# Kernel tuning notes

Hardware: AMD Instinct MI355X
Metric: run time of the kernel (lower is better)

Reference implementation:

```python
import jax, jax.numpy as jnp
import numpy as np

NUM_LAYERS = 3

def setup_inputs() -> dict:
    key = jax.random.key(0)
    ks = jax.random.split(key, 16)
    B = 8192
    NU, NI, D = 60000, 40000, 64
    N = NU + NI
    T_TRAIN, T_MAX = 128, 256
    E = 1600000
    return {
        "user_indices": jax.random.randint(ks[0], (B,), 0, NU, dtype=jnp.int32).astype(jnp.int64),
        "item_indices": jax.random.randint(ks[1], (B,), 0, NI, dtype=jnp.int32).astype(jnp.int64),
        "time_diffs": jax.random.randint(ks[2], (B,), 0, T_TRAIN, dtype=jnp.int32).astype(jnp.int64),
        "user_trends": jax.random.normal(ks[3], (B, T_TRAIN), dtype=jnp.float32),
        "item_trends": jax.random.normal(ks[4], (B, T_TRAIN), dtype=jnp.float32),
        "user_emb_table": 0.01 * jax.random.normal(ks[5], (NU, D), dtype=jnp.float32),
        "item_emb_table": 0.01 * jax.random.normal(ks[6], (NI, D), dtype=jnp.float32),
        "user_time_table": 0.01 * jax.random.normal(ks[7], (NU, T_MAX), dtype=jnp.float32),
        "item_time_table": 0.01 * jax.random.normal(ks[8], (NI, T_MAX), dtype=jnp.float32),
        "W1": 0.05 * jax.random.normal(ks[9], (T_TRAIN, 32), dtype=jnp.float32),
        "b1": jnp.zeros((32,), dtype=jnp.float32),
        "W2": 0.05 * jax.random.normal(ks[10], (32, T_MAX - T_TRAIN), dtype=jnp.float32),
        "b2": jnp.zeros((T_MAX - T_TRAIN,), dtype=jnp.float32),
        "edge_src": jax.random.randint(ks[11], (E,), 0, N, dtype=jnp.int32),
        "edge_dst": jax.random.randint(ks[12], (E,), 0, N, dtype=jnp.int32),
    }


def _graph_forward(user_emb_table, item_emb_table, edge_src, edge_dst):
    # LightGCN-style: mean of in-neighbor source features, num_layers hops,
    # then average over [input, layer1, ..., layerL] embeddings.
    N = user_emb_table.shape[0] + item_emb_table.shape[0]
    emb = jnp.concatenate([user_emb_table, item_emb_table], axis=0)  # [N, D]
    deg = jax.ops.segment_sum(jnp.ones_like(edge_dst, dtype=emb.dtype), edge_dst, num_segments=N)
    inv_deg = jnp.where(deg > 0, 1.0 / jnp.maximum(deg, 1.0), 0.0)[:, None]  # zero for isolated nodes (DGL mean -> 0)
    acc = emb
    cur = emb
    for _ in range(NUM_LAYERS):
        msgs = cur[edge_src]  # [E, D] gather
        summed = jax.ops.segment_sum(msgs, edge_dst, num_segments=N)
        cur = summed * inv_deg
        acc = acc + cur
    final = acc / jnp.asarray(NUM_LAYERS + 1, emb.dtype)
    return final[: user_emb_table.shape[0]], final[user_emb_table.shape[0]:]


def _mlp(t, W1, b1, W2, b2):
    # Linear->ReLU->Dropout(eval: identity)->Linear
    h = jax.nn.relu(t @ W1 + b1)
    return h @ W2 + b2


def reference(user_indices, item_indices, time_diffs, user_trends, item_trends,
              user_emb_table, item_emb_table, user_time_table, item_time_table,
              W1, b1, W2, b2, edge_src, edge_dst):
    user_embeddings, item_embeddings = _graph_forward(user_emb_table, item_emb_table, edge_src, edge_dst)
    ue = user_embeddings[user_indices]  # [B, D]
    ie = item_embeddings[item_indices]  # [B, D]
    global_match = jnp.sum(ue * ie, axis=-1)  # [B]

    ute = user_time_table[user_indices]  # [B, T_MAX]
    ite = item_time_table[item_indices]
    ut = jnp.concatenate([user_trends, _mlp(user_trends, W1, b1, W2, b2)], axis=1)  # [B, T_MAX]
    it = jnp.concatenate([item_trends, _mlp(item_trends, W1, b1, W2, b2)], axis=1)
    user_time_match = jnp.sum(ute * ut, axis=-1)
    item_time_match = jnp.sum(ite * it, axis=-1)

    B = user_indices.shape[0]
    ue0 = user_emb_table[user_indices]
    ie0 = item_emb_table[item_indices]
    reg_loss = 0.5 * (jnp.sum(ue0 ** 2) + jnp.sum(ie0 ** 2) + jnp.sum(ute ** 2) + jnp.sum(ite ** 2)) / float(B)

    return (jax.nn.sigmoid(global_match), jax.nn.sigmoid(user_time_match + item_time_match), reg_loss)
```

## Files before the change

### kernel.cpp

```cpp
#include <hip/hip_runtime.h>
#include <math.h>


__device__ __forceinline__ float bf2f(unsigned short h) {
    return __uint_as_float((unsigned)h << 16);
}
__device__ __forceinline__ unsigned short f2bf(float f) {
    unsigned u = __float_as_uint(f);
    return (unsigned short)((u + 0x7fffu + ((u >> 16) & 1u)) >> 16);
}


__global__ __launch_bounds__(256) void conv_kernel(
    const float* __restrict__ utab, const float* __restrict__ itab,
    unsigned short* __restrict__ fb, int total, int uElems,
    int* __restrict__ cursor2, float* __restrict__ out2, int convBlocks) {
    if ((int)blockIdx.x == convBlocks) {
        cursor2[threadIdx.x] = 0;
        if (threadIdx.x == 0) out2[0] = 0.0f;
        return;
    }
    int i = (blockIdx.x * 256 + threadIdx.x) * 4;
    if (i >= total + 64) return;
    ushort4 o;
    if (i < total) {
        const float* srcp = (i < uElems) ? (utab + i) : (itab + (i - uElems));
        float4 v = *(const float4*)srcp;
        o.x = f2bf(v.x); o.y = f2bf(v.y); o.z = f2bf(v.z); o.w = f2bf(v.w);
    } else {
        o.x = 0; o.y = 0; o.z = 0; o.w = 0;
    }
    *(ushort4*)(fb + i) = o;
}


__global__ __launch_bounds__(256) void bin2_kernel(
    const int* __restrict__ src, const int* __restrict__ dst,
    int* __restrict__ cursor2, unsigned long long* __restrict__ pairs2,
    int E, int cap) {
    __shared__ int lcnt[256];
    __shared__ int lbase[256];
    int tid = threadIdx.x;
    int base = blockIdx.x * 4096;
    lcnt[tid] = 0;
    __syncthreads();
    #pragma unroll
    for (int i = 0; i < 16; ++i) {
        int e = base + i * 256 + tid;
        if (e < E) atomicAdd(&lcnt[dst[e] >> 9], 1);
    }
    __syncthreads();
    int c = lcnt[tid];
    lbase[tid] = (c > 0) ? atomicAdd(&cursor2[tid], c) : 0;
    __syncthreads();
    lcnt[tid] = 0;
    __syncthreads();
    #pragma unroll
    for (int i = 0; i < 16; ++i) {
        int e = base + i * 256 + tid;
        if (e < E) {
            int d = dst[e], s = src[e];
            int b = d >> 9;
            int r = lbase[b] + atomicAdd(&lcnt[b], 1);
            if (r < cap)
                pairs2[(size_t)b * cap + r] =
                    ((unsigned long long)(unsigned)d << 32) | (unsigned)s;
        }
    }
}


__global__ __launch_bounds__(256) void sort3_kernel(
    const unsigned long long* __restrict__ pairs2,
    const int* __restrict__ cursor2,
    float* __restrict__ invd, int* __restrict__ csr, int NODE_N, int cap) {
    __shared__ int lcnt[512];
    int bin = blockIdx.x;
    int nodebase = bin << 9;
    int n = cursor2[bin];
    if (n > cap) n = cap;
    const unsigned long long* p = pairs2 + (size_t)bin * cap;
    int tid = threadIdx.x;

    lcnt[tid] = 0;
    lcnt[tid + 256] = 0;
    __syncthreads();
    for (int i = tid; i < n; i += 256) {
        unsigned long long pr = p[i];
        int d = (int)(pr >> 32), s = (int)(pr & 0xffffffffu);
        int pos = atomicAdd(&lcnt[d - nodebase], 1);
        if (pos < 64) csr[(size_t)d * 64 + pos] = s;
    }
    __syncthreads();
    #pragma unroll
    for (int t = 0; t < 2; ++t) {
        int j = tid + t * 256;
        int node = nodebase + j;
        if (node <= NODE_N) {
            int own = lcnt[j];
            invd[node] = (own > 0) ? 1.0f / (float)own : 0.0f;
            int d0 = (own < 64) ? own : 64;
            int pend = (own <= 32) ? 32 : 64;
            int* row = csr + (size_t)node * 64;
            for (int k = d0; k < pend; ++k) row[k] = NODE_N;
        }
    }
}


#define GATHER4(buf, sv, gx, gy, gz, gw_)                                  \
    {                                                                      \
        ushort4 v_ = *(const ushort4*)((buf) + (size_t)(sv) * 64 + 4 * cL);\
        gx += bf2f(v_.x); gy += bf2f(v_.y);                                \
        gz += bf2f(v_.z); gw_ += bf2f(v_.w);                               \
    }
#define RED2(x) { x += __shfl_xor(x, 16, 64); x += __shfl_xor(x, 32, 64); }

__global__ __launch_bounds__(256) void prop_kernel(
    const unsigned short* __restrict__ cur,
    const int* __restrict__ csr, const float* __restrict__ invd,
    unsigned short* __restrict__ nxt, int NP1) {
    int w = (blockIdx.x * blockDim.x + threadIdx.x) >> 6;
    int lane = threadIdx.x & 63;
    int n0 = 2 * w, n1 = 2 * w + 1;
    if (n0 >= NP1) return;
    bool v1 = (n1 < NP1);
    int n1c = v1 ? n1 : n0;
    int g = lane >> 4;
    int cL = lane & 15;
    const int* c0 = csr + (size_t)n0 * 64;
    const int* c1 = csr + (size_t)n1c * 64;
    float inv0 = invd[n0];
    float inv1 = v1 ? invd[n1c] : 0.f;
    int s0 = c0[g], s1 = c0[4 + g], s2 = c0[8 + g], s3 = c0[12 + g];
    int t0 = c1[g], t1 = c1[4 + g], t2 = c1[8 + g], t3 = c1[12 + g];

    float ax = 0.f, ay = 0.f, az = 0.f, aw = 0.f;
    float bx = 0.f, by = 0.f, bz = 0.f, bw = 0.f;
    float ex = 0.f, ey = 0.f, ez = 0.f, ew = 0.f;
    float fx = 0.f, fy = 0.f, fz = 0.f, fw = 0.f;
    GATHER4(cur, s0, ax, ay, az, aw);
    GATHER4(cur, s1, bx, by, bz, bw);
    GATHER4(cur, t0, ex, ey, ez, ew);
    GATHER4(cur, t1, fx, fy, fz, fw);
    GATHER4(cur, s2, ax, ay, az, aw);
    GATHER4(cur, s3, bx, by, bz, bw);
    GATHER4(cur, t2, ex, ey, ez, ew);
    GATHER4(cur, t3, fx, fy, fz, fw);

    int deg0 = (inv0 > 0.f) ? (int)(1.0f / inv0 + 0.5f) : 0;
    int deg1 = (inv1 > 0.f) ? (int)(1.0f / inv1 + 0.5f) : 0;
    if (deg0 > 16) {
        int s4 = c0[16 + g], s5 = c0[20 + g], s6 = c0[24 + g], s7 = c0[28 + g];
        GATHER4(cur, s4, ax, ay, az, aw);
        GATHER4(cur, s5, bx, by, bz, bw);
        GATHER4(cur, s6, ax, ay, az, aw);
        GATHER4(cur, s7, bx, by, bz, bw);
    }
    if (deg1 > 16) {
        int t4 = c1[16 + g], t5 = c1[20 + g], t6 = c1[24 + g], t7 = c1[28 + g];
        GATHER4(cur, t4, ex, ey, ez, ew);
        GATHER4(cur, t5, fx, fy, fz, fw);
        GATHER4(cur, t6, ex, ey, ez, ew);
        GATHER4(cur, t7, fx, fy, fz, fw);
    }
    if (deg0 > 32) {
        #pragma unroll
        for (int pb = 32; pb < 64; pb += 8) {
            int u0 = c0[pb + g], u1 = c0[pb + 4 + g];
            GATHER4(cur, u0, ax, ay, az, aw);
            GATHER4(cur, u1, bx, by, bz, bw);
        }
    }
    if (deg1 > 32) {
        #pragma unroll
        for (int pb = 32; pb < 64; pb += 8) {
            int u0 = c1[pb + g], u1 = c1[pb + 4 + g];
            GATHER4(cur, u0, ex, ey, ez, ew);
            GATHER4(cur, u1, fx, fy, fz, fw);
        }
    }
    ax += bx; ay += by; az += bz; aw += bw;
    ex += fx; ey += fy; ez += fz; ew += fw;
    RED2(ax); RED2(ay); RED2(az); RED2(aw);
    RED2(ex); RED2(ey); RED2(ez); RED2(ew);
    if (g == 0) {
        ushort4 o;
        o.x = f2bf(ax * inv0); o.y = f2bf(ay * inv0);
        o.z = f2bf(az * inv0); o.w = f2bf(aw * inv0);
        *(ushort4*)(nxt + (size_t)n0 * 64 + 4 * cL) = o;
    } else if (g == 1 && v1) {
        ushort4 o;
        o.x = f2bf(ex * inv1); o.y = f2bf(ey * inv1);
        o.z = f2bf(ez * inv1); o.w = f2bf(ew * inv1);
        *(ushort4*)(nxt + (size_t)n1c * 64 + 4 * cL) = o;
    }
}


__global__ __launch_bounds__(256) void timedot_kernel(
    const int* __restrict__ uidx, const int* __restrict__ iidx,
    const float* __restrict__ utr, const float* __restrict__ itr,
    const float* __restrict__ utt, const float* __restrict__ itt,
    const float* __restrict__ utab, const float* __restrict__ itab,
    const float* __restrict__ W1, const float* __restrict__ b1,
    const float* __restrict__ W2, const float* __restrict__ b2,
    const unsigned short* __restrict__ fb2,
    const unsigned short* __restrict__ fb1l,
    const int* __restrict__ csr, const float* __restrict__ invd,
    float* __restrict__ out0, float* __restrict__ out1,
    float* __restrict__ out2, int B, int NU, float regScale) {
    __shared__ float sh[4][320];
    __shared__ float rsh[4];
    int wid = threadIdx.x >> 6, lane = threadIdx.x & 63;
    int b = blockIdx.x * 4 + wid;
    bool valid = (b < B);
    int bb = valid ? b : (B - 1);

    float* tu = sh[wid];
    float* ti = tu + 128;
    float* hu = ti + 128;
    float* hi = hu + 32;

    tu[lane]      = utr[(size_t)bb * 128 + lane];
    tu[lane + 64] = utr[(size_t)bb * 128 + 64 + lane];
    ti[lane]      = itr[(size_t)bb * 128 + lane];
    ti[lane + 64] = itr[(size_t)bb * 128 + 64 + lane];
    __syncthreads();

    {
        int j = lane & 31;
        const float* t = (lane < 32) ? tu : ti;
        float acc = b1[j];
        #pragma unroll 8
        for (int k = 0; k < 128; ++k) acc += t[k] * W1[k * 32 + j];
        float* h = (lane < 32) ? hu : hi;
        h[j] = fmaxf(acc, 0.0f);
    }
    __syncthreads();

    float mu0 = b2[lane], mu1 = b2[64 + lane];
    float mi0 = b2[lane], mi1 = b2[64 + lane];
    #pragma unroll 8
    for (int j = 0; j < 32; ++j) {
        float w0 = W2[j * 128 + lane], w1 = W2[j * 128 + 64 + lane];
        float huj = hu[j], hij = hi[j];
        mu0 += huj * w0; mu1 += huj * w1;
        mi0 += hij * w0; mi1 += hij * w1;
    }

    int u = uidx[bb], it = iidx[bb];
    const float* uterow = utt + (size_t)u * 256;
    const float* iterow = itt + (size_t)it * 256;
    float ute0 = uterow[lane], ute1 = uterow[64 + lane], ute2 = uterow[128 + lane], ute3 = uterow[192 + lane];
    float ite0 = iterow[lane], ite1 = iterow[64 + lane], ite2 = iterow[128 + lane], ite3 = iterow[192 + lane];

    float utm = ute0 * tu[lane] + ute1 * tu[64 + lane] + ute2 * mu0 + ute3 * mu1;
    float itm = ite0 * ti[lane] + ite1 * ti[64 + lane] + ite2 * mi0 + ite3 * mi1;

    float regA = ute0 * ute0 + ute1 * ute1 + ute2 * ute2 + ute3 * ute3
               + ite0 * ite0 + ite1 * ite1 + ite2 * ite2 + ite3 * ite3;

    int g = lane >> 4;
    int cL = lane & 15;
    int nu_node = u;
    int ni_node = NU + it;
    const int* cu = csr + (size_t)nu_node * 64;
    const int* ci = csr + (size_t)ni_node * 64;
    float invU = invd[nu_node];
    float invI = invd[ni_node];
    int s0 = cu[g], s1 = cu[4 + g], s2 = cu[8 + g], s3 = cu[12 + g];
    int s4 = cu[16 + g], s5 = cu[20 + g], s6 = cu[24 + g], s7 = cu[28 + g];
    int t0 = ci[g], t1 = ci[4 + g], t2 = ci[8 + g], t3 = ci[12 + g];
    int t4 = ci[16 + g], t5 = ci[20 + g], t6 = ci[24 + g], t7 = ci[28 + g];

    float ax = 0.f, ay = 0.f, az = 0.f, aw = 0.f;
    float bx = 0.f, by = 0.f, bz = 0.f, bw = 0.f;
    float ex = 0.f, ey = 0.f, ez = 0.f, ew = 0.f;
    float fx = 0.f, fy = 0.f, fz = 0.f, fw = 0.f;
    GATHER4(fb2, s0, ax, ay, az, aw);
    GATHER4(fb2, s1, bx, by, bz, bw);
    GATHER4(fb2, t0, ex, ey, ez, ew);
    GATHER4(fb2, t1, fx, fy, fz, fw);
    GATHER4(fb2, s2, ax, ay, az, aw);
    GATHER4(fb2, s3, bx, by, bz, bw);
    GATHER4(fb2, t2, ex, ey, ez, ew);
    GATHER4(fb2, t3, fx, fy, fz, fw);
    GATHER4(fb2, s4, ax, ay, az, aw);
    GATHER4(fb2, s5, bx, by, bz, bw);
    GATHER4(fb2, t4, ex, ey, ez, ew);
    GATHER4(fb2, t5, fx, fy, fz, fw);
    GATHER4(fb2, s6, ax, ay, az, aw);
    GATHER4(fb2, s7, bx, by, bz, bw);
    GATHER4(fb2, t6, ex, ey, ez, ew);
    GATHER4(fb2, t7, fx, fy, fz, fw);

    int degU = (invU > 0.f) ? (int)(1.0f / invU + 0.5f) : 0;
    int degI = (invI > 0.f) ? (int)(1.0f / invI + 0.5f) : 0;
    if (degU > 32) {
        #pragma unroll
        for (int pb = 32; pb < 64; pb += 8) {
            int u0 = cu[pb + g], u1 = cu[pb + 4 + g];
            GATHER4(fb2, u0, ax, ay, az, aw);
            GATHER4(fb2, u1, bx, by, bz, bw);
        }
    }
    if (degI > 32) {
        #pragma unroll
        for (int pb = 32; pb < 64; pb += 8) {
            int u0 = ci[pb + g], u1 = ci[pb + 4 + g];
            GATHER4(fb2, u0, ex, ey, ez, ew);
            GATHER4(fb2, u1, fx, fy, fz, fw);
        }
    }
    ax += bx; ay += by; az += bz; aw += bw;
    ex += fx; ey += fy; ez += fz; ew += fw;
    RED2(ax); RED2(ay); RED2(az); RED2(aw);
    RED2(ex); RED2(ey); RED2(ez); RED2(ew);

    float4 l0u = *(const float4*)(utab + (size_t)nu_node * 64 + 4 * cL);
    float4 l0i = *(const float4*)(itab + (size_t)it * 64 + 4 * cL);
    ushort4 l1u = *(const ushort4*)(fb1l + (size_t)nu_node * 64 + 4 * cL);
    ushort4 l1i = *(const ushort4*)(fb1l + (size_t)ni_node * 64 + 4 * cL);
    ushort4 l2u = *(const ushort4*)(fb2 + (size_t)nu_node * 64 + 4 * cL);
    ushort4 l2i = *(const ushort4*)(fb2 + (size_t)ni_node * 64 + 4 * cL);

    float ue0_ = l0u.x + bf2f(l1u.x) + bf2f(l2u.x) + ax * invU;
    float ue1_ = l0u.y + bf2f(l1u.y) + bf2f(l2u.y) + ay * invU;
    float ue2_ = l0u.z + bf2f(l1u.z) + bf2f(l2u.z) + az * invU;
    float ue3_ = l0u.w + bf2f(l1u.w) + bf2f(l2u.w) + aw * invU;
    float ie0_ = l0i.x + bf2f(l1i.x) + bf2f(l2i.x) + ex * invI;
    float ie1_ = l0i.y + bf2f(l1i.y) + bf2f(l2i.y) + ey * invI;
    float ie2_ = l0i.z + bf2f(l1i.z) + bf2f(l2i.z) + ez * invI;
    float ie3_ = l0i.w + bf2f(l1i.w) + bf2f(l2i.w) + ew * invI;

    float dv = ue0_ * ie0_ + ue1_ * ie1_ + ue2_ * ie2_ + ue3_ * ie3_;
    float regB = l0u.x * l0u.x + l0u.y * l0u.y + l0u.z * l0u.z + l0u.w * l0u.w
               + l0i.x * l0i.x + l0i.y * l0i.y + l0i.z * l0i.z + l0i.w * l0i.w;
    float reg = regA + 0.25f * regB;

    float s = utm + itm;
    for (int o = 32; o; o >>= 1) {
        s   += __shfl_down(s, o, 64);
        reg += __shfl_down(reg, o, 64);
        dv  += __shfl_down(dv, o, 64);
    }
    if (lane == 0) {
        if (valid) {
            out0[b] = 1.0f / (1.0f + expf(-dv * (1.0f / 64.0f)));
            out1[b] = 1.0f / (1.0f + expf(-s));
        }
        rsh[wid] = valid ? reg : 0.0f;
    }
    __syncthreads();
    if (threadIdx.x == 0) {
        float blocksum = rsh[0] + rsh[1] + rsh[2] + rsh[3];
        atomicAdd(out2, blocksum * regScale);
    }
}

extern "C" void kernel_launch(void* const* d_in, const int* in_sizes, int n_in,
                              void* d_out, int out_size, void* d_ws, size_t ws_size,
                              hipStream_t stream) {
    const int*   uidx = (const int*)d_in[0];
    const int*   iidx = (const int*)d_in[1];
    const float* utr  = (const float*)d_in[3];
    const float* itr  = (const float*)d_in[4];
    const float* utab = (const float*)d_in[5];
    const float* itab = (const float*)d_in[6];
    const float* utt  = (const float*)d_in[7];
    const float* itt  = (const float*)d_in[8];
    const float* W1   = (const float*)d_in[9];
    const float* b1   = (const float*)d_in[10];
    const float* W2   = (const float*)d_in[11];
    const float* b2   = (const float*)d_in[12];
    const int*   esrc = (const int*)d_in[13];
    const int*   edst = (const int*)d_in[14];

    const int B  = in_sizes[0];
    const int H  = in_sizes[10];
    const int TT = in_sizes[9] / H;
    const int TM = TT + in_sizes[12];
    const int NU = in_sizes[7] / TM;
    const int NI = in_sizes[8] / TM;
    const int N  = NU + NI;
    const int E  = in_sizes[13];
    const int D  = 64;
    const int nbin = (N + 1 + 511) >> 9;
    const int cap = 12288;

    char* ws = (char*)d_ws;
    size_t o = 0;
    auto carve = [&](size_t bytes) -> char* {
        char* p = ws + o;
        o = (o + bytes + 255) & ~(size_t)255;
        return p;
    };
    unsigned short* fb0 = (unsigned short*)carve((size_t)(N + 1) * D * sizeof(unsigned short));
    size_t fb1Bytes = (size_t)(N + 1) * D * sizeof(unsigned short);
    size_t p2Bytes  = (size_t)256 * cap * sizeof(unsigned long long);
    unsigned short* fb1 = (unsigned short*)carve(fb1Bytes > p2Bytes ? fb1Bytes : p2Bytes);
    float* invd    = (float*)carve((size_t)(N + 2) * sizeof(float));
    int*   csr     = (int*)  carve((size_t)(N + 1) * 64 * sizeof(int));
    int*   cursor2 = (int*)  carve(256 * sizeof(int));
    (void)ws_size;

    unsigned long long* pairs2 = (unsigned long long*)fb1;

    float* out0 = (float*)d_out;
    float* out1 = out0 + B;
    float* out2 = out1 + B;

    const int convBlocks = ((N * D + 64) / 4 + 255) / 256;
    conv_kernel<<<convBlocks + 1, 256, 0, stream>>>(
        utab, itab, fb0, N * D, NU * D, cursor2, out2, convBlocks);

    bin2_kernel<<<(E + 4095) / 4096, 256, 0, stream>>>(esrc, edst, cursor2, pairs2, E, cap);
    sort3_kernel<<<nbin, 256, 0, stream>>>(pairs2, cursor2, invd, csr, N, cap);

    const int NP1 = N + 1;
    const int prop_waves = (NP1 + 1) / 2;
    const int prop_blocks = (prop_waves * 64 + 255) / 256;
    prop_kernel<<<prop_blocks, 256, 0, stream>>>(fb0, csr, invd, fb1, NP1);
    prop_kernel<<<prop_blocks, 256, 0, stream>>>(fb1, csr, invd, fb0, NP1);

    timedot_kernel<<<(B + 3) / 4, 256, 0, stream>>>(
        uidx, iidx, utr, itr, utt, itt, utab, itab, W1, b1, W2, b2,
        fb0, fb1, csr, invd, out0, out1, out2, B, NU, 0.5f / (float)B);
}
```

Baseline: 154.5 us.

## Split tail kernel into separate graph-dot and time-MLP blocks

The final kernel now launches twice as many blocks. Even blocks do the third-layer neighbour gather and the embedding dot product. Odd blocks do the trend MLP, the time-table dot products and the regularisation sum. Loads in the time path are hoisted ahead of the MLP, and the reg term now reads the full user/item embedding rows per lane instead of the 4-wide slice. The intent is more parallelism and latency hiding in the gather-heavy tail, at the cost of extra blocks and duplicated index loads.

```diff
diff --git a/kernel.cpp b/kernel.cpp
--- a/kernel.cpp
+++ b/kernel.cpp
@@ -15,12 +15,13 @@
     const float* __restrict__ utab, const float* __restrict__ itab,
     unsigned short* __restrict__ fb, int total, int uElems,
     int* __restrict__ cursor2, float* __restrict__ out2, int convBlocks) {
-    if ((int)blockIdx.x == convBlocks) {
+    int bid = blockIdx.x;
+    if (bid == convBlocks) {
         cursor2[threadIdx.x] = 0;
         if (threadIdx.x == 0) out2[0] = 0.0f;
         return;
     }
-    int i = (blockIdx.x * 256 + threadIdx.x) * 4;
+    int i = (bid * 256 + threadIdx.x) * 4;
     if (i >= total + 64) return;
     ushort4 o;
     if (i < total) {
@@ -198,34 +199,124 @@
 }
 
 
-__global__ __launch_bounds__(256) void timedot_kernel(
+__global__ __launch_bounds__(256) void tail_kernel(
     const int* __restrict__ uidx, const int* __restrict__ iidx,
+    const unsigned short* __restrict__ fb2,
+    const unsigned short* __restrict__ fb1l,
+    const int* __restrict__ csr, const float* __restrict__ invd,
     const float* __restrict__ utr, const float* __restrict__ itr,
     const float* __restrict__ utt, const float* __restrict__ itt,
     const float* __restrict__ utab, const float* __restrict__ itab,
     const float* __restrict__ W1, const float* __restrict__ b1,
     const float* __restrict__ W2, const float* __restrict__ b2,
-    const unsigned short* __restrict__ fb2,
-    const unsigned short* __restrict__ fb1l,
-    const int* __restrict__ csr, const float* __restrict__ invd,
     float* __restrict__ out0, float* __restrict__ out1,
     float* __restrict__ out2, int B, int NU, float regScale) {
     __shared__ float sh[4][320];
     __shared__ float rsh[4];
     int wid = threadIdx.x >> 6, lane = threadIdx.x & 63;
-    int b = blockIdx.x * 4 + wid;
+    int pairIdx = blockIdx.x >> 1;
+
+    if ((blockIdx.x & 1) == 0) {
+        int b = pairIdx * 4 + wid;
+        if (b >= B) return;
+        int g = lane >> 4;
+        int cL = lane & 15;
+        int u = uidx[b], it = iidx[b];
+        int nodeU = u, nodeI = NU + it;
+        const int* cu = csr + (size_t)nodeU * 64;
+        const int* ci = csr + (size_t)nodeI * 64;
+        float invU = invd[nodeU];
+        float invI = invd[nodeI];
+        float4 l0u = *(const float4*)(utab + (size_t)nodeU * 64 + 4 * cL);
+        float4 l0i = *(const float4*)(itab + (size_t)it * 64 + 4 * cL);
+        ushort4 l1u = *(const ushort4*)(fb1l + (size_t)nodeU * 64 + 4 * cL);
+        ushort4 l1i = *(const ushort4*)(fb1l + (size_t)nodeI * 64 + 4 * cL);
+        ushort4 l2u = *(const ushort4*)(fb2 + (size_t)nodeU * 64 + 4 * cL);
+        ushort4 l2i = *(const ushort4*)(fb2 + (size_t)nodeI * 64 + 4 * cL);
+        int s0 = cu[g],      s1 = cu[4 + g],  s2 = cu[8 + g],  s3 = cu[12 + g];
+        int s4 = cu[16 + g], s5 = cu[20 + g], s6 = cu[24 + g], s7 = cu[28 + g];
+        int t0 = ci[g],      t1 = ci[4 + g],  t2 = ci[8 + g],  t3 = ci[12 + g];
+        int t4 = ci[16 + g], t5 = ci[20 + g], t6 = ci[24 + g], t7 = ci[28 + g];
+
+        float ax = 0.f, ay = 0.f, az = 0.f, aw = 0.f;
+        float bx = 0.f, by = 0.f, bz = 0.f, bw = 0.f;
+        float ex = 0.f, ey = 0.f, ez = 0.f, ew = 0.f;
+        float fx = 0.f, fy = 0.f, fz = 0.f, fw = 0.f;
+        GATHER4(fb2, s0, ax, ay, az, aw);
+        GATHER4(fb2, s1, bx, by, bz, bw);
+        GATHER4(fb2, t0, ex, ey, ez, ew);
+        GATHER4(fb2, t1, fx, fy, fz, fw);
+        GATHER4(fb2, s2, ax, ay, az, aw);
+        GATHER4(fb2, s3, bx, by, bz, bw);
+        GATHER4(fb2, t2, ex, ey, ez, ew);
+        GATHER4(fb2, t3, fx, fy, fz, fw);
+        GATHER4(fb2, s4, ax, ay, az, aw);
+        GATHER4(fb2, s5, bx, by, bz, bw);
+        GATHER4(fb2, t4, ex, ey, ez, ew);
+        GATHER4(fb2, t5, fx, fy, fz, fw);
+        GATHER4(fb2, s6, ax, ay, az, aw);
+        GATHER4(fb2, s7, bx, by, bz, bw);
+        GATHER4(fb2, t6, ex, ey, ez, ew);
+        GATHER4(fb2, t7, fx, fy, fz, fw);
+
+        int degU = (invU > 0.f) ? (int)(1.0f / invU + 0.5f) : 0;
+        int degI = (invI > 0.f) ? (int)(1.0f / invI + 0.5f) : 0;
+        if (degU > 32) {
+            #pragma unroll
+            for (int pb = 32; pb < 64; pb += 8) {
+                int u0 = cu[pb + g], u1 = cu[pb + 4 + g];
+                GATHER4(fb2, u0, ax, ay, az, aw);
+                GATHER4(fb2, u1, bx, by, bz, bw);
+            }
+        }
+        if (degI > 32) {
+            #pragma unroll
+            for (int pb = 32; pb < 64; pb += 8) {
+                int u0 = ci[pb + g], u1 = ci[pb + 4 + g];
+                GATHER4(fb2, u0, ex, ey, ez, ew);
+                GATHER4(fb2, u1, fx, fy, fz, fw);
+            }
+        }
+        ax += bx; ay += by; az += bz; aw += bw;
+        ex += fx; ey += fy; ez += fz; ew += fw;
+        RED2(ax); RED2(ay); RED2(az); RED2(aw);
+        RED2(ex); RED2(ey); RED2(ez); RED2(ew);
+
+        float ue0_ = l0u.x + bf2f(l1u.x) + bf2f(l2u.x) + ax * invU;
+        float ue1_ = l0u.y + bf2f(l1u.y) + bf2f(l2u.y) + ay * invU;
+        float ue2_ = l0u.z + bf2f(l1u.z) + bf2f(l2u.z) + az * invU;
+        float ue3_ = l0u.w + bf2f(l1u.w) + bf2f(l2u.w) + aw * invU;
+        float ie0_ = l0i.x + bf2f(l1i.x) + bf2f(l2i.x) + ex * invI;
+        float ie1_ = l0i.y + bf2f(l1i.y) + bf2f(l2i.y) + ey * invI;
+        float ie2_ = l0i.z + bf2f(l1i.z) + bf2f(l2i.z) + ez * invI;
+        float ie3_ = l0i.w + bf2f(l1i.w) + bf2f(l2i.w) + ew * invI;
+
+        float dv = ue0_ * ie0_ + ue1_ * ie1_ + ue2_ * ie2_ + ue3_ * ie3_;
+        for (int o = 32; o; o >>= 1) dv += __shfl_down(dv, o, 64);
+        if (lane == 0)
+            out0[b] = 1.0f / (1.0f + expf(-dv * (1.0f / 64.0f)));
+        return;
+    }
+
+    int b = pairIdx * 4 + wid;
     bool valid = (b < B);
     int bb = valid ? b : (B - 1);
+    int u = uidx[bb], it = iidx[bb];
+
+    const float* uterow = utt + (size_t)u * 256;
+    const float* iterow = itt + (size_t)it * 256;
+    float ute0 = uterow[lane], ute1 = uterow[64 + lane], ute2 = uterow[128 + lane], ute3 = uterow[192 + lane];
+    float ite0 = iterow[lane], ite1 = iterow[64 + lane], ite2 = iterow[128 + lane], ite3 = iterow[192 + lane];
+    float ue0 = utab[(size_t)u * 64 + lane], ie0 = itab[(size_t)it * 64 + lane];
+    float tu0 = utr[(size_t)bb * 128 + lane], tu1 = utr[(size_t)bb * 128 + 64 + lane];
+    float ti0 = itr[(size_t)bb * 128 + lane], ti1 = itr[(size_t)bb * 128 + 64 + lane];
 
     float* tu = sh[wid];
     float* ti = tu + 128;
     float* hu = ti + 128;
     float* hi = hu + 32;
-
-    tu[lane]      = utr[(size_t)bb * 128 + lane];
-    tu[lane + 64] = utr[(size_t)bb * 128 + 64 + lane];
-    ti[lane]      = itr[(size_t)bb * 128 + lane];
-    ti[lane + 64] = itr[(size_t)bb * 128 + 64 + lane];
+    tu[lane] = tu0; tu[lane + 64] = tu1;
+    ti[lane] = ti0; ti[lane + 64] = ti1;
     __syncthreads();
 
     {
@@ -249,107 +340,20 @@
         mi0 += hij * w0; mi1 += hij * w1;
     }
 
-    int u = uidx[bb], it = iidx[bb];
-    const float* uterow = utt + (size_t)u * 256;
-    const float* iterow = itt + (size_t)it * 256;
-    float ute0 = uterow[lane], ute1 = uterow[64 + lane], ute2 = uterow[128 + lane], ute3 = uterow[192 + lane];
-    float ite0 = iterow[lane], ite1 = iterow[64 + lane], ite2 = iterow[128 + lane], ite3 = iterow[192 + lane];
-
-    float utm = ute0 * tu[lane] + ute1 * tu[64 + lane] + ute2 * mu0 + ute3 * mu1;
-    float itm = ite0 * ti[lane] + ite1 * ti[64 + lane] + ite2 * mi0 + ite3 * mi1;
-
-    float regA = ute0 * ute0 + ute1 * ute1 + ute2 * ute2 + ute3 * ute3
-               + ite0 * ite0 + ite1 * ite1 + ite2 * ite2 + ite3 * ite3;
-
-    int g = lane >> 4;
-    int cL = lane & 15;
-    int nu_node = u;
-    int ni_node = NU + it;
-    const int* cu = csr + (size_t)nu_node * 64;
-    const int* ci = csr + (size_t)ni_node * 64;
-    float invU = invd[nu_node];
-    float invI = invd[ni_node];
-    int s0 = cu[g], s1 = cu[4 + g], s2 = cu[8 + g], s3 = cu[12 + g];
-    int s4 = cu[16 + g], s5 = cu[20 + g], s6 = cu[24 + g], s7 = cu[28 + g];
-    int t0 = ci[g], t1 = ci[4 + g], t2 = ci[8 + g], t3 = ci[12 + g];
-    int t4 = ci[16 + g], t5 = ci[20 + g], t6 = ci[24 + g], t7 = ci[28 + g];
-
-    float ax = 0.f, ay = 0.f, az = 0.f, aw = 0.f;
-    float bx = 0.f, by = 0.f, bz = 0.f, bw = 0.f;
-    float ex = 0.f, ey = 0.f, ez = 0.f, ew = 0.f;
-    float fx = 0.f, fy = 0.f, fz = 0.f, fw = 0.f;
-    GATHER4(fb2, s0, ax, ay, az, aw);
-    GATHER4(fb2, s1, bx, by, bz, bw);
-    GATHER4(fb2, t0, ex, ey, ez, ew);
-    GATHER4(fb2, t1, fx, fy, fz, fw);
-    GATHER4(fb2, s2, ax, ay, az, aw);
-    GATHER4(fb2, s3, bx, by, bz, bw);
-    GATHER4(fb2, t2, ex, ey, ez, ew);
-    GATHER4(fb2, t3, fx, fy, fz, fw);
-    GATHER4(fb2, s4, ax, ay, az, aw);
-    GATHER4(fb2, s5, bx, by, bz, bw);
-    GATHER4(fb2, t4, ex, ey, ez, ew);
-    GATHER4(fb2, t5, fx, fy, fz, fw);
-    GATHER4(fb2, s6, ax, ay, az, aw);
-    GATHER4(fb2, s7, bx, by, bz, bw);
-    GATHER4(fb2, t6, ex, ey, ez, ew);
-    GATHER4(fb2, t7, fx, fy, fz, fw);
-
-    int degU = (invU > 0.f) ? (int)(1.0f / invU + 0.5f) : 0;
-    int degI = (invI > 0.f) ? (int)(1.0f / invI + 0.5f) : 0;
-    if (degU > 32) {
-        #pragma unroll
-        for (int pb = 32; pb < 64; pb += 8) {
-            int u0 = cu[pb + g], u1 = cu[pb + 4 + g];
-            GATHER4(fb2, u0, ax, ay, az, aw);
-            GATHER4(fb2, u1, bx, by, bz, bw);
-        }
-    }
-    if (degI > 32) {
-        #pragma unroll
-        for (int pb = 32; pb < 64; pb += 8) {
-            int u0 = ci[pb + g], u1 = ci[pb + 4 + g];
-            GATHER4(fb2, u0, ex, ey, ez, ew);
-            GATHER4(fb2, u1, fx, fy, fz, fw);
-        }
-    }
-    ax += bx; ay += by; az += bz; aw += bw;
-    ex += fx; ey += fy; ez += fz; ew += fw;
-    RED2(ax); RED2(ay); RED2(az); RED2(aw);
-    RED2(ex); RED2(ey); RED2(ez); RED2(ew);
-
-    float4 l0u = *(const float4*)(utab + (size_t)nu_node * 64 + 4 * cL);
-    float4 l0i = *(const float4*)(itab + (size_t)it * 64 + 4 * cL);
-    ushort4 l1u = *(const ushort4*)(fb1l + (size_t)nu_node * 64 + 4 * cL);
-    ushort4 l1i = *(const ushort4*)(fb1l + (size_t)ni_node * 64 + 4 * cL);
-    ushort4 l2u = *(const ushort4*)(fb2 + (size_t)nu_node * 64 + 4 * cL);
-    ushort4 l2i = *(const ushort4*)(fb2 + (size_t)ni_node * 64 + 4 * cL);
-
-    float ue0_ = l0u.x + bf2f(l1u.x) + bf2f(l2u.x) + ax * invU;
-    float ue1_ = l0u.y + bf2f(l1u.y) + bf2f(l2u.y) + ay * invU;
-    float ue2_ = l0u.z + bf2f(l1u.z) + bf2f(l2u.z) + az * invU;
-    float ue3_ = l0u.w + bf2f(l1u.w) + bf2f(l2u.w) + aw * invU;
-    float ie0_ = l0i.x + bf2f(l1i.x) + bf2f(l2i.x) + ex * invI;
-    float ie1_ = l0i.y + bf2f(l1i.y) + bf2f(l2i.y) + ey * invI;
-    float ie2_ = l0i.z + bf2f(l1i.z) + bf2f(l2i.z) + ez * invI;
-    float ie3_ = l0i.w + bf2f(l1i.w) + bf2f(l2i.w) + ew * invI;
-
-    float dv = ue0_ * ie0_ + ue1_ * ie1_ + ue2_ * ie2_ + ue3_ * ie3_;
-    float regB = l0u.x * l0u.x + l0u.y * l0u.y + l0u.z * l0u.z + l0u.w * l0u.w
-               + l0i.x * l0i.x + l0i.y * l0i.y + l0i.z * l0i.z + l0i.w * l0i.w;
-    float reg = regA + 0.25f * regB;
+    float utm = ute0 * tu0 + ute1 * tu1 + ute2 * mu0 + ute3 * mu1;
+    float itm = ite0 * ti0 + ite1 * ti1 + ite2 * mi0 + ite3 * mi1;
+
+    float reg = ute0 * ute0 + ute1 * ute1 + ute2 * ute2 + ute3 * ute3
+              + ite0 * ite0 + ite1 * ite1 + ite2 * ite2 + ite3 * ite3
+              + ue0 * ue0 + ie0 * ie0;
 
     float s = utm + itm;
     for (int o = 32; o; o >>= 1) {
         s   += __shfl_down(s, o, 64);
         reg += __shfl_down(reg, o, 64);
-        dv  += __shfl_down(dv, o, 64);
     }
     if (lane == 0) {
-        if (valid) {
-            out0[b] = 1.0f / (1.0f + expf(-dv * (1.0f / 64.0f)));
-            out1[b] = 1.0f / (1.0f + expf(-s));
-        }
+        if (valid) out1[b] = 1.0f / (1.0f + expf(-s));
         rsh[wid] = valid ? reg : 0.0f;
     }
     __syncthreads();
@@ -424,7 +428,9 @@
     prop_kernel<<<prop_blocks, 256, 0, stream>>>(fb0, csr, invd, fb1, NP1);
     prop_kernel<<<prop_blocks, 256, 0, stream>>>(fb1, csr, invd, fb0, NP1);
 
-    timedot_kernel<<<(B + 3) / 4, 256, 0, stream>>>(
-        uidx, iidx, utr, itr, utt, itt, utab, itab, W1, b1, W2, b2,
-        fb0, fb1, csr, invd, out0, out1, out2, B, NU, 0.5f / (float)B);
-}
+    const int pairBlocks = (B + 3) / 4;
+    tail_kernel<<<2 * pairBlocks, 256, 0, stream>>>(
+        uidx, iidx, fb0, fb1, csr, invd,
+        utr, itr, utt, itt, utab, itab, W1, b1, W2, b2,
+        out0, out1, out2, B, NU, 0.5f / (float)B);
+}
```

After: 157.1 us (median of 2 runs). Within noise of the previous version (+1.7%).
